# Kernel tuning notes

Measured on AMD Instinct MI355X. Metric: run time of the kernel, lower is better.

## Reference

```python
import jax, jax.numpy as jnp
import numpy as np

NUM_HEADS = 16
D_MODEL = 1024
NEG_INF = -1e30


def setup_inputs() -> dict:
    key = jax.random.key(0)
    ks = jax.random.split(key, 7)
    B, S, D = 2, 2048, D_MODEL
    scale = 1.0 / np.sqrt(D)
    return {
        "queries": jax.random.normal(ks[0], (B, S, D), dtype=jnp.float32),
        "keys": jax.random.normal(ks[1], (B, S, D), dtype=jnp.float32),
        "values": jax.random.normal(ks[2], (B, S, D), dtype=jnp.float32),
        "Wq": jax.random.normal(ks[3], (D, D), dtype=jnp.float32) * scale,
        "Wk": jax.random.normal(ks[4], (D, D), dtype=jnp.float32) * scale,
        "Wv": jax.random.normal(ks[5], (D, D), dtype=jnp.float32) * scale,
        "Wo": jax.random.normal(ks[6], (D, D), dtype=jnp.float32) * scale,
    }


def _split_heads(x, h):
    # [B, S, D] -> [B, h, S, D/h]
    B, S, D = x.shape
    return x.reshape(B, S, h, D // h).transpose(0, 2, 1, 3)


def reference(queries, keys, values, Wq, Wk, Wv, Wo):
    h = NUM_HEADS
    q = _split_heads(queries @ Wq, h)  # [B, h, S, dh]
    k = _split_heads(keys @ Wk, h)
    v = _split_heads(values @ Wv, h)
    dh = q.shape[-1]
    scores = jnp.einsum("bhqd,bhkd->bhqk", q, k) / jnp.sqrt(jnp.float32(dh))
    # original quirk: exactly-zero scores are masked to -1e30 before softmax
    scores = jnp.where(scores == 0, NEG_INF, scores)
    attn = jax.nn.softmax(scores, axis=-1)
    out = jnp.einsum("bhqk,bhkd->bhqd", attn, v)  # [B, h, S, dh]
    B, _, S, _ = out.shape
    out = out.transpose(0, 2, 1, 3).reshape(B, S, h * dh)
    return out @ Wo
```

## Files before the change

### kernel.cpp

```cpp
#include <hip/hip_runtime.h>

typedef unsigned short u16;
typedef short bf16x8 __attribute__((ext_vector_type(8)));
typedef float f32x4 __attribute__((ext_vector_type(4)));
typedef float f32x16 __attribute__((ext_vector_type(16)));

namespace {

constexpr int kB = 2, kS = 2048, kD = 1024, kH = 16, kDh = 64;
constexpr float kC2 = 0.125f * 1.44269504088896341f;

__device__ inline u16 f32_bf16(float f) {
    unsigned u = __float_as_uint(f);
    u += 0x7FFFu + ((u >> 16) & 1u);
    return (u16)(u >> 16);
}

__device__ inline float fast_exp2(float x) {
    float r;
    asm("v_exp_f32 %0, %1" : "=v"(r) : "v"(x));
    return r;
}

__device__ inline unsigned cvtpk(float a, float b) {
    unsigned r;
    asm("v_cvt_pk_bf16_f32 %0, %1, %2" : "=v"(r) : "v"(a), "v"(b));
    return r;
}

__device__ inline void plswap(unsigned& a, unsigned& b) {
    asm("v_permlane32_swap_b32 %0, %1" : "+v"(a), "+v"(b));
}

__device__ inline void gl_lds16(const void* g, void* l) {
    __builtin_amdgcn_global_load_lds(
        (const __attribute__((address_space(1))) void*)g,
        (__attribute__((address_space(3))) void*)l, 16, 0, 0);
}

__device__ inline int swz8(int l) {
    return ((l & 3) ^ ((l >> 2) & 3) ^ ((l >> 4) & 3)) * 8;
}

__global__ __launch_bounds__(256) void prep(
    const float* __restrict__ s0, const float* __restrict__ s1,
    const float* __restrict__ s2,
    u16* __restrict__ d0, u16* __restrict__ d1, u16* __restrict__ d2,
    const float* __restrict__ W0, const float* __restrict__ W1,
    const float* __restrict__ W2, const float* __restrict__ W3,
    u16* __restrict__ T0, u16* __restrict__ T1,
    u16* __restrict__ T2, u16* __restrict__ T3)
{
    const int y = blockIdx.y;
    if (y < 3) {
        const float* src = y == 0 ? s0 : (y == 1 ? s1 : s2);
        u16* dst = y == 0 ? d0 : (y == 1 ? d1 : d2);
        const int i = blockIdx.x * 256 + threadIdx.x;
        const float4* s4 = (const float4*)src;
        float4 a = s4[2 * i], b = s4[2 * i + 1];
        uint4 o;
        o.x = (unsigned)f32_bf16(a.x) | ((unsigned)f32_bf16(a.y) << 16);
        o.y = (unsigned)f32_bf16(a.z) | ((unsigned)f32_bf16(a.w) << 16);
        o.z = (unsigned)f32_bf16(b.x) | ((unsigned)f32_bf16(b.y) << 16);
        o.w = (unsigned)f32_bf16(b.z) | ((unsigned)f32_bf16(b.w) << 16);
        ((uint4*)dst)[i] = o;
        return;
    }
    if (blockIdx.x >= 256) return;
    const int z = y - 3;
    const float* W = z == 0 ? W0 : (z == 1 ? W1 : (z == 2 ? W2 : W3));
    u16* Wt = z == 0 ? T0 : (z == 1 ? T1 : (z == 2 ? T2 : T3));
    const float sc = (z == 0) ? kC2 : 1.0f;

    __shared__ __attribute__((aligned(16))) u16 T[64][65];
    const int t = threadIdx.x;
    const int n0 = (blockIdx.x & 15) * 64, k0 = (blockIdx.x >> 4) * 64;
    const int r = t >> 4, c4 = (t & 15) * 4;
#pragma unroll
    for (int it = 0; it < 4; ++it) {
        const int rr = r + 16 * it;
        float4 v = *(const float4*)(W + (size_t)(k0 + rr) * kD + n0 + c4);
        T[rr][c4 + 0] = f32_bf16(v.x * sc);
        T[rr][c4 + 1] = f32_bf16(v.y * sc);
        T[rr][c4 + 2] = f32_bf16(v.z * sc);
        T[rr][c4 + 3] = f32_bf16(v.w * sc);
    }
    __syncthreads();
#pragma unroll
    for (int it = 0; it < 4; ++it) {
        const int nn = r + 16 * it;
        uint2 pk;
        pk.x = (unsigned)T[c4 + 0][nn] | ((unsigned)T[c4 + 1][nn] << 16);
        pk.y = (unsigned)T[c4 + 2][nn] | ((unsigned)T[c4 + 3][nn] << 16);
        *(uint2*)(Wt + (size_t)(n0 + nn) * kD + k0 + c4) = pk;
    }
}

__global__ __launch_bounds__(256) void vtrans(
    const u16* __restrict__ V, u16* __restrict__ Vt)
{
    __shared__ __attribute__((aligned(16))) u16 T[64][65];
    const int t = threadIdx.x;
    const int s0 = blockIdx.x * 64;
    const int bh = blockIdx.y, b = bh >> 4, h = bh & 15;
    const int rr = t >> 3, c0 = (t & 7) * 8;
    union { u16 u[8]; uint4 v4; } buf;
#pragma unroll
    for (int p = 0; p < 2; ++p) {
        const int s = rr + 32 * p;
        buf.v4 = *(const uint4*)(V + (size_t)(b * kS + s0 + s) * kD + h * kDh + c0);
#pragma unroll
        for (int i = 0; i < 8; ++i) T[c0 + i][s] = buf.u[i];
    }
    __syncthreads();
#pragma unroll
    for (int p = 0; p < 2; ++p) {
        const int d = rr + 32 * p;
#pragma unroll
        for (int i = 0; i < 8; ++i) buf.u[i] = T[d][c0 + i];
        *(uint4*)(Vt + (size_t)(bh * kDh + d) * kS + s0 + c0) = buf.v4;
    }
}

template <bool F32OUT>
__device__ inline void gemm128_body(
    const u16* __restrict__ A, const u16* __restrict__ Wt,
    void* __restrict__ Cout, int M, int N, int K, int bx, int by)
{
    __shared__ __attribute__((aligned(16))) u16 As[128 * 32];
    __shared__ __attribute__((aligned(16))) u16 Bs[128 * 32];
    const int t = threadIdx.x, w = t >> 6, l = t & 63;
    const int quad = l >> 4, c = l & 15;
    const int wm = w >> 1, wn = w & 1;
    const int m0 = by * 128, n0 = bx * 128;
    const int lr = l >> 2, lc = swz8(l);
    const int xc = ((quad ^ (c & 3) ^ ((c >> 2) & 3))) * 8;

    const u16* ga0 = A  + (size_t)(m0 + w * 32 + lr) * K + lc;
    const u16* ga1 = A  + (size_t)(m0 + w * 32 + 16 + lr) * K + lc;
    const u16* gb0 = Wt + (size_t)(n0 + w * 32 + lr) * K + lc;
    const u16* gb1 = Wt + (size_t)(n0 + w * 32 + 16 + lr) * K + lc;
    u16* la0 = &As[(w * 32) * 32];
    u16* la1 = &As[(w * 32 + 16) * 32];
    u16* lb0 = &Bs[(w * 32) * 32];
    u16* lb1 = &Bs[(w * 32 + 16) * 32];

    f32x4 acc[4][4];
#pragma unroll
    for (int mi = 0; mi < 4; ++mi)
#pragma unroll
        for (int nj = 0; nj < 4; ++nj) acc[mi][nj] = 0;

    for (int k0 = 0; k0 < K; k0 += 32) {
        gl_lds16(ga0 + k0, la0);
        gl_lds16(ga1 + k0, la1);
        gl_lds16(gb0 + k0, lb0);
        gl_lds16(gb1 + k0, lb1);
        __syncthreads();
        bf16x8 af[4], bf[4];
#pragma unroll
        for (int mi = 0; mi < 4; ++mi)
            af[mi] = *(const bf16x8*)&As[(wm * 64 + mi * 16 + c) * 32 + xc];
#pragma unroll
        for (int nj = 0; nj < 4; ++nj)
            bf[nj] = *(const bf16x8*)&Bs[(wn * 64 + nj * 16 + c) * 32 + xc];
#pragma unroll
        for (int mi = 0; mi < 4; ++mi)
#pragma unroll
            for (int nj = 0; nj < 4; ++nj)
                acc[mi][nj] = __builtin_amdgcn_mfma_f32_16x16x32_bf16(
                    af[mi], bf[nj], acc[mi][nj], 0, 0, 0);
        __syncthreads();
    }

#pragma unroll
    for (int mi = 0; mi < 4; ++mi)
#pragma unroll
        for (int nj = 0; nj < 4; ++nj)
#pragma unroll
            for (int r = 0; r < 4; ++r) {
                const size_t row = m0 + wm * 64 + mi * 16 + quad * 4 + r;
                const size_t col = n0 + wn * 64 + nj * 16 + c;
                if (F32OUT)
                    ((float*)Cout)[row * N + col] = acc[mi][nj][r];
                else
                    ((u16*)Cout)[row * N + col] = f32_bf16(acc[mi][nj][r]);
            }
}

__global__ __launch_bounds__(256) void gemm_qkv(
    const u16* __restrict__ A0, const u16* __restrict__ A1,
    const u16* __restrict__ A2,
    const u16* __restrict__ W0, const u16* __restrict__ W1,
    const u16* __restrict__ W2,
    u16* __restrict__ C0, u16* __restrict__ C1, u16* __restrict__ C2)
{
    const int z = blockIdx.z;
    const u16* A  = z == 0 ? A0 : (z == 1 ? A1 : A2);
    const u16* Wt = z == 0 ? W0 : (z == 1 ? W1 : W2);
    u16* C = z == 0 ? C0 : (z == 1 ? C1 : C2);
    gemm128_body<false>(A, Wt, C, kB * kS, kD, kD, blockIdx.x, blockIdx.y);
}

__global__ __launch_bounds__(256) void gemm_out(
    const u16* __restrict__ A, const u16* __restrict__ Wt,
    float* __restrict__ C)
{
    __shared__ __attribute__((aligned(16))) u16 As[64 * 32];
    __shared__ __attribute__((aligned(16))) u16 Bs[128 * 32];
    const int N = kD, K = kD;
    const int t = threadIdx.x, w = t >> 6, l = t & 63;
    const int quad = l >> 4, c = l & 15;
    const int wm = w >> 1, wn = w & 1;
    const int m0 = blockIdx.y * 64, n0 = blockIdx.x * 128;
    const int lr = l >> 2, lc = swz8(l);
    const int xc = ((quad ^ (c & 3) ^ ((c >> 2) & 3))) * 8;

    const u16* ga  = A  + (size_t)(m0 + w * 16 + lr) * K + lc;
    const u16* gb0 = Wt + (size_t)(n0 + w * 16 + lr) * K + lc;
    const u16* gb1 = Wt + (size_t)(n0 + 64 + w * 16 + lr) * K + lc;
    u16* la  = &As[(w * 16) * 32];
    u16* lb0 = &Bs[(w * 16) * 32];
    u16* lb1 = &Bs[(64 + w * 16) * 32];

    f32x4 acc[2][4];
#pragma unroll
    for (int mi = 0; mi < 2; ++mi)
#pragma unroll
        for (int nj = 0; nj < 4; ++nj) acc[mi][nj] = 0;

    for (int k0 = 0; k0 < K; k0 += 32) {
        gl_lds16(ga + k0, la);
        gl_lds16(gb0 + k0, lb0);
        gl_lds16(gb1 + k0, lb1);
        __syncthreads();
        bf16x8 af[2], bf[4];
#pragma unroll
        for (int mi = 0; mi < 2; ++mi)
            af[mi] = *(const bf16x8*)&As[(wm * 32 + mi * 16 + c) * 32 + xc];
#pragma unroll
        for (int nj = 0; nj < 4; ++nj)
            bf[nj] = *(const bf16x8*)&Bs[(wn * 64 + nj * 16 + c) * 32 + xc];
#pragma unroll
        for (int mi = 0; mi < 2; ++mi)
#pragma unroll
            for (int nj = 0; nj < 4; ++nj)
                acc[mi][nj] = __builtin_amdgcn_mfma_f32_16x16x32_bf16(
                    af[mi], bf[nj], acc[mi][nj], 0, 0, 0);
        __syncthreads();
    }

#pragma unroll
    for (int mi = 0; mi < 2; ++mi)
#pragma unroll
        for (int nj = 0; nj < 4; ++nj)
#pragma unroll
            for (int r = 0; r < 4; ++r) {
                const size_t row = m0 + wm * 32 + mi * 16 + quad * 4 + r;
                const size_t col = n0 + wn * 64 + nj * 16 + c;
                C[row * N + col] = acc[mi][nj][r];
            }
}

__global__ __launch_bounds__(256) void attn(
    const u16* __restrict__ Q, const u16* __restrict__ K,
    const u16* __restrict__ Vt, u16* __restrict__ AO)
{
    __shared__ __attribute__((aligned(16))) u16 KsA[64 * 64];
    __shared__ __attribute__((aligned(16))) u16 KsB[64 * 64];
    __shared__ __attribute__((aligned(16))) u16 VtA[64 * 64];
    __shared__ __attribute__((aligned(16))) u16 VtB[64 * 64];

    const int t = threadIdx.x, w = t >> 6, l = t & 63;
    const int half = l >> 5, m = l & 31;
    const int wgid = blockIdx.x;
    const int xcd = wgid & 7, idx = wgid >> 3;
    const int bh = xcd + 8 * (idx & 3);
    const int q0 = (idx >> 2) * 128;
    const int b = bh >> 4, h = bh & 15;
    const int sr = l >> 3;
    const int sc = (l & 7) ^ sr;

    const size_t kbase = (size_t)(b * kS) * kD + h * kDh;
    const size_t vbase = (size_t)bh * kDh * kS;

    auto stage = [&](int kt, u16* KsP, u16* VtP) {
#pragma unroll
        for (int i = 0; i < 2; ++i) {
            const int R0 = w * 16 + i * 8;
            gl_lds16(K + kbase + (size_t)(kt * 64 + R0 + sr) * kD + sc * 8,
                     &KsP[R0 * 64]);
            gl_lds16(Vt + vbase + (size_t)(R0 + sr) * kS + kt * 64 + sc * 8,
                     &VtP[R0 * 64]);
        }
    };

    stage(0, KsA, VtA);

    bf16x8 qf[4];
    {
        const u16* qp = Q + (size_t)(b * kS + q0 + w * 32 + m) * kD
                        + h * kDh + half * 8;
#pragma unroll
        for (int ch = 0; ch < 4; ++ch)
            qf[ch] = *(const bf16x8*)(qp + ch * 16);
    }

    bf16x8 ones;
#pragma unroll
    for (int i = 0; i < 8; ++i) ones[i] = (short)0x3F80;

    f32x16 o0 = 0, o1 = 0;
    f32x16 ol = 0;

    __syncthreads();

    auto compute = [&](const u16* KsP, const u16* VtP) {
        f32x16 s0 = 0, s1 = 0;
        __builtin_amdgcn_s_setprio(1);
#pragma unroll
        for (int ch = 0; ch < 4; ++ch) {
            const int xo = ((2 * ch + half) ^ (m & 7)) * 8;
            const bf16x8 kf0 = *(const bf16x8*)&KsP[(m) * 64 + xo];
            const bf16x8 kf1 = *(const bf16x8*)&KsP[(32 + m) * 64 + xo];
            s0 = __builtin_amdgcn_mfma_f32_32x32x16_bf16(kf0, qf[ch], s0, 0, 0, 0);
            s1 = __builtin_amdgcn_mfma_f32_32x32x16_bf16(kf1, qf[ch], s1, 0, 0, 0);
        }
        __builtin_amdgcn_s_setprio(0);
#pragma unroll
        for (int r = 0; r < 16; ++r) {
            s0[r] = fast_exp2(s0[r]);
            s1[r] = fast_exp2(s1[r]);
        }
        __builtin_amdgcn_s_setprio(1);
#pragma unroll
        for (int ts = 0; ts < 4; ++ts) {
            const int rb = (ts & 1) * 8;
            unsigned c0, c1, c2, c3;
            if (ts < 2) {
                c0 = cvtpk(s0[rb + 0], s0[rb + 1]);
                c1 = cvtpk(s0[rb + 2], s0[rb + 3]);
                c2 = cvtpk(s0[rb + 4], s0[rb + 5]);
                c3 = cvtpk(s0[rb + 6], s0[rb + 7]);
            } else {
                c0 = cvtpk(s1[rb + 0], s1[rb + 1]);
                c1 = cvtpk(s1[rb + 2], s1[rb + 3]);
                c2 = cvtpk(s1[rb + 4], s1[rb + 5]);
                c3 = cvtpk(s1[rb + 6], s1[rb + 7]);
            }
            plswap(c0, c2);
            plswap(c1, c3);
            union { unsigned u[4]; bf16x8 v; } pb;
            pb.u[0] = c0; pb.u[1] = c1; pb.u[2] = c2; pb.u[3] = c3;
            const int xo = ((2 * ts + half) ^ (m & 7)) * 8;
            const bf16x8 vf0 = *(const bf16x8*)&VtP[(m) * 64 + xo];
            const bf16x8 vf1 = *(const bf16x8*)&VtP[(32 + m) * 64 + xo];
            o0 = __builtin_amdgcn_mfma_f32_32x32x16_bf16(vf0, pb.v, o0, 0, 0, 0);
            o1 = __builtin_amdgcn_mfma_f32_32x32x16_bf16(vf1, pb.v, o1, 0, 0, 0);
            ol = __builtin_amdgcn_mfma_f32_32x32x16_bf16(ones, pb.v, ol, 0, 0, 0);
        }
        __builtin_amdgcn_s_setprio(0);
    };

    constexpr int NT = kS / 64;
#pragma unroll 1
    for (int kt = 0; kt < NT; kt += 2) {
        if (kt + 1 < NT) stage(kt + 1, KsB, VtB);
        compute(KsA, VtA);
        __syncthreads();
        if (kt + 2 < NT) stage(kt + 2, KsA, VtA);
        compute(KsB, VtB);
        __syncthreads();
    }

    const float inv = 1.0f / ol[0];

    u16* ob = w == 0 ? KsA : (w == 1 ? KsB : (w == 2 ? VtA : VtB));
#pragma unroll
    for (int r = 0; r < 4; ++r) {
        uint2 p0, p1;
        p0.x = cvtpk(o0[4 * r + 0] * inv, o0[4 * r + 1] * inv);
        p0.y = cvtpk(o0[4 * r + 2] * inv, o0[4 * r + 3] * inv);
        p1.x = cvtpk(o1[4 * r + 0] * inv, o1[4 * r + 1] * inv);
        p1.y = cvtpk(o1[4 * r + 2] * inv, o1[4 * r + 3] * inv);
        *(uint2*)&ob[m * 64 + ((r ^ (m & 7)) << 3) + 4 * half] = p0;
        *(uint2*)&ob[m * 64 + (((4 + r) ^ (m & 7)) << 3) + 4 * half] = p1;
    }
    const size_t obase = (size_t)(b * kS + q0 + w * 32) * kD + h * kDh;
#pragma unroll
    for (int i = 0; i < 4; ++i) {
        const int q = l >> 1;
        const int tt = (l & 1) + i * 2;
        uint4 dd = *(const uint4*)&ob[q * 64 + ((tt ^ (q & 7)) << 3)];
        *(uint4*)(AO + obase + (size_t)q * kD + tt * 8) = dd;
    }
}

}

extern "C" void kernel_launch(void* const* d_in, const int* in_sizes, int n_in,
                              void* d_out, int out_size, void* d_ws, size_t ws_size,
                              hipStream_t stream)
{
    const float* q_in = (const float*)d_in[0];
    const float* k_in = (const float*)d_in[1];
    const float* v_in = (const float*)d_in[2];
    const float* Wq   = (const float*)d_in[3];
    const float* Wk   = (const float*)d_in[4];
    const float* Wv   = (const float*)d_in[5];
    const float* Wo   = (const float*)d_in[6];

    u16* ws = (u16*)d_ws;
    const size_t M1 = 1u << 20;
    u16* xq  = ws;
    u16* xk  = ws + 4 * M1;
    u16* xv  = ws + 8 * M1;
    u16* Wtq = ws + 12 * M1;
    u16* Wtk = ws + 13 * M1;
    u16* Wtv = ws + 14 * M1;
    u16* Wto = ws + 15 * M1;
    u16* Qp  = ws + 16 * M1;
    u16* Kp  = ws + 20 * M1;
    u16* Vp  = ws + 24 * M1;
    u16* AO  = ws + 28 * M1;
    u16* Vtg = xq;

    hipLaunchKernelGGL(prep, dim3(2048, 7), dim3(256), 0, stream,
                       q_in, k_in, v_in, xq, xk, xv,
                       Wq, Wk, Wv, Wo, Wtq, Wtk, Wtv, Wto);

    hipLaunchKernelGGL(gemm_qkv, dim3(8, 32, 3), dim3(256), 0, stream,
                       xq, xk, xv, Wtq, Wtk, Wtv, Qp, Kp, Vp);

    hipLaunchKernelGGL(vtrans, dim3(32, 32), dim3(256), 0, stream, Vp, Vtg);

    hipLaunchKernelGGL(attn, dim3(512), dim3(256), 0, stream, Qp, Kp, Vtg, AO);

    hipLaunchKernelGGL(gemm_out, dim3(8, 64), dim3(256), 0, stream,
                       AO, Wto, (float*)d_out);
}
```

Measured before the change: 217.2 us.

## Fuse V transpose into QKV GEMM epilogue and reswizzle attention LDS tiles

The separate vtrans kernel is removed. The V-projection blocks of gemm_qkv now transpose their accumulator tile through shared memory and write V directly in the [bh, d, s] layout that attention reads. This saves one launch and one round trip of V through global memory, at the cost of extra LDS in the GEMM, which may lower its occupancy. The attention kernel's K/Vt LDS swizzle also now XORs in the row-group bits, meant to reduce bank conflicts on the fragment reads.

```diff
diff --git a/kernel.cpp b/kernel.cpp
--- a/kernel.cpp
+++ b/kernel.cpp
@@ -96,43 +96,25 @@
     }
 }
 
-__global__ __launch_bounds__(256) void vtrans(
-    const u16* __restrict__ V, u16* __restrict__ Vt)
-{
-    __shared__ __attribute__((aligned(16))) u16 T[64][65];
-    const int t = threadIdx.x;
-    const int s0 = blockIdx.x * 64;
-    const int bh = blockIdx.y, b = bh >> 4, h = bh & 15;
-    const int rr = t >> 3, c0 = (t & 7) * 8;
-    union { u16 u[8]; uint4 v4; } buf;
-#pragma unroll
-    for (int p = 0; p < 2; ++p) {
-        const int s = rr + 32 * p;
-        buf.v4 = *(const uint4*)(V + (size_t)(b * kS + s0 + s) * kD + h * kDh + c0);
-#pragma unroll
-        for (int i = 0; i < 8; ++i) T[c0 + i][s] = buf.u[i];
-    }
-    __syncthreads();
-#pragma unroll
-    for (int p = 0; p < 2; ++p) {
-        const int d = rr + 32 * p;
-#pragma unroll
-        for (int i = 0; i < 8; ++i) buf.u[i] = T[d][c0 + i];
-        *(uint4*)(Vt + (size_t)(bh * kDh + d) * kS + s0 + c0) = buf.v4;
-    }
-}
-
-template <bool F32OUT>
-__device__ inline void gemm128_body(
-    const u16* __restrict__ A, const u16* __restrict__ Wt,
-    void* __restrict__ Cout, int M, int N, int K, int bx, int by)
+__global__ __launch_bounds__(256) void gemm_qkv(
+    const u16* __restrict__ A0, const u16* __restrict__ A1,
+    const u16* __restrict__ A2,
+    const u16* __restrict__ W0, const u16* __restrict__ W1,
+    const u16* __restrict__ W2,
+    u16* __restrict__ C0, u16* __restrict__ C1, u16* __restrict__ Vt)
 {
     __shared__ __attribute__((aligned(16))) u16 As[128 * 32];
     __shared__ __attribute__((aligned(16))) u16 Bs[128 * 32];
+    __shared__ __attribute__((aligned(16))) u16 Tt[64][136];
+    const int N = kD, K = kD;
+    const int z = blockIdx.z;
+    const u16* A  = z == 0 ? A0 : (z == 1 ? A1 : A2);
+    const u16* Wt = z == 0 ? W0 : (z == 1 ? W1 : W2);
+
     const int t = threadIdx.x, w = t >> 6, l = t & 63;
     const int quad = l >> 4, c = l & 15;
     const int wm = w >> 1, wn = w & 1;
-    const int m0 = by * 128, n0 = bx * 128;
+    const int m0 = blockIdx.y * 128, n0 = blockIdx.x * 128;
     const int lr = l >> 2, lc = swz8(l);
     const int xc = ((quad ^ (c & 3) ^ ((c >> 2) & 3))) * 8;
 
@@ -173,33 +155,45 @@
         __syncthreads();
     }
 
-#pragma unroll
-    for (int mi = 0; mi < 4; ++mi)
-#pragma unroll
-        for (int nj = 0; nj < 4; ++nj)
-#pragma unroll
-            for (int r = 0; r < 4; ++r) {
-                const size_t row = m0 + wm * 64 + mi * 16 + quad * 4 + r;
-                const size_t col = n0 + wn * 64 + nj * 16 + c;
-                if (F32OUT)
-                    ((float*)Cout)[row * N + col] = acc[mi][nj][r];
-                else
-                    ((u16*)Cout)[row * N + col] = f32_bf16(acc[mi][nj][r]);
-            }
-}
-
-__global__ __launch_bounds__(256) void gemm_qkv(
-    const u16* __restrict__ A0, const u16* __restrict__ A1,
-    const u16* __restrict__ A2,
-    const u16* __restrict__ W0, const u16* __restrict__ W1,
-    const u16* __restrict__ W2,
-    u16* __restrict__ C0, u16* __restrict__ C1, u16* __restrict__ C2)
-{
-    const int z = blockIdx.z;
-    const u16* A  = z == 0 ? A0 : (z == 1 ? A1 : A2);
-    const u16* Wt = z == 0 ? W0 : (z == 1 ? W1 : W2);
-    u16* C = z == 0 ? C0 : (z == 1 ? C1 : C2);
-    gemm128_body<false>(A, Wt, C, kB * kS, kD, kD, blockIdx.x, blockIdx.y);
+    if (z < 2) {
+        u16* C = z == 0 ? C0 : C1;
+#pragma unroll
+        for (int mi = 0; mi < 4; ++mi)
+#pragma unroll
+            for (int nj = 0; nj < 4; ++nj)
+#pragma unroll
+                for (int r = 0; r < 4; ++r) {
+                    const size_t row = m0 + wm * 64 + mi * 16 + quad * 4 + r;
+                    const size_t col = n0 + wn * 64 + nj * 16 + c;
+                    C[row * N + col] = f32_bf16(acc[mi][nj][r]);
+                }
+        return;
+    }
+    const int srow = m0 & 2047;
+    const int bbase = (m0 >> 11) << 4;
+#pragma unroll 1
+    for (int p = 0; p < 2; ++p) {
+        if (wn == p) {
+#pragma unroll
+            for (int mi = 0; mi < 4; ++mi)
+#pragma unroll
+                for (int nj = 0; nj < 4; ++nj)
+#pragma unroll
+                    for (int r = 0; r < 4; ++r)
+                        Tt[nj * 16 + c][wm * 64 + mi * 16 + quad * 4 + r] =
+                            f32_bf16(acc[mi][nj][r]);
+        }
+        __syncthreads();
+        const size_t vb = (size_t)(bbase + blockIdx.x * 2 + p) * (kDh * kS);
+        const int s8 = t & 15, dbase = t >> 4;
+#pragma unroll
+        for (int dd = 0; dd < 4; ++dd) {
+            const int d = dbase + dd * 16;
+            uint4 v = *(const uint4*)&Tt[d][s8 * 8];
+            *(uint4*)(Vt + vb + (size_t)d * kS + srow + s8 * 8) = v;
+        }
+        __syncthreads();
+    }
 }
 
 __global__ __launch_bounds__(256) void gemm_out(
@@ -279,7 +273,6 @@
     const int q0 = (idx >> 2) * 128;
     const int b = bh >> 4, h = bh & 15;
     const int sr = l >> 3;
-    const int sc = (l & 7) ^ sr;
 
     const size_t kbase = (size_t)(b * kS) * kD + h * kDh;
     const size_t vbase = (size_t)bh * kDh * kS;
@@ -288,6 +281,7 @@
 #pragma unroll
         for (int i = 0; i < 2; ++i) {
             const int R0 = w * 16 + i * 8;
+            const int sc = (l & 7) ^ sr ^ (w * 2 + i);
             gl_lds16(K + kbase + (size_t)(kt * 64 + R0 + sr) * kD + sc * 8,
                      &KsP[R0 * 64]);
             gl_lds16(Vt + vbase + (size_t)(R0 + sr) * kS + kt * 64 + sc * 8,
@@ -320,9 +314,9 @@
         __builtin_amdgcn_s_setprio(1);
 #pragma unroll
         for (int ch = 0; ch < 4; ++ch) {
-            const int xo = ((2 * ch + half) ^ (m & 7)) * 8;
+            const int xo = ((2 * ch + half) ^ (m & 7) ^ (m >> 3)) * 8;
             const bf16x8 kf0 = *(const bf16x8*)&KsP[(m) * 64 + xo];
-            const bf16x8 kf1 = *(const bf16x8*)&KsP[(32 + m) * 64 + xo];
+            const bf16x8 kf1 = *(const bf16x8*)&KsP[(32 + m) * 64 + (xo ^ 32)];
             s0 = __builtin_amdgcn_mfma_f32_32x32x16_bf16(kf0, qf[ch], s0, 0, 0, 0);
             s1 = __builtin_amdgcn_mfma_f32_32x32x16_bf16(kf1, qf[ch], s1, 0, 0, 0);
         }
@@ -352,9 +346,9 @@
             plswap(c1, c3);
             union { unsigned u[4]; bf16x8 v; } pb;
             pb.u[0] = c0; pb.u[1] = c1; pb.u[2] = c2; pb.u[3] = c3;
-            const int xo = ((2 * ts + half) ^ (m & 7)) * 8;
+            const int xo = ((2 * ts + half) ^ (m & 7) ^ (m >> 3)) * 8;
             const bf16x8 vf0 = *(const bf16x8*)&VtP[(m) * 64 + xo];
-            const bf16x8 vf1 = *(const bf16x8*)&VtP[(32 + m) * 64 + xo];
+            const bf16x8 vf1 = *(const bf16x8*)&VtP[(32 + m) * 64 + (xo ^ 32)];
             o0 = __builtin_amdgcn_mfma_f32_32x32x16_bf16(vf0, pb.v, o0, 0, 0, 0);
             o1 = __builtin_amdgcn_mfma_f32_32x32x16_bf16(vf1, pb.v, o1, 0, 0, 0);
             ol = __builtin_amdgcn_mfma_f32_32x32x16_bf16(ones, pb.v, ol, 0, 0, 0);
@@ -421,20 +415,17 @@
     u16* Wto = ws + 15 * M1;
     u16* Qp  = ws + 16 * M1;
     u16* Kp  = ws + 20 * M1;
-    u16* Vp  = ws + 24 * M1;
+    u16* Vt  = ws + 24 * M1;
     u16* AO  = ws + 28 * M1;
-    u16* Vtg = xq;
 
     hipLaunchKernelGGL(prep, dim3(2048, 7), dim3(256), 0, stream,
                        q_in, k_in, v_in, xq, xk, xv,
                        Wq, Wk, Wv, Wo, Wtq, Wtk, Wtv, Wto);
 
     hipLaunchKernelGGL(gemm_qkv, dim3(8, 32, 3), dim3(256), 0, stream,
-                       xq, xk, xv, Wtq, Wtk, Wtv, Qp, Kp, Vp);
-
-    hipLaunchKernelGGL(vtrans, dim3(32, 32), dim3(256), 0, stream, Vp, Vtg);
-
-    hipLaunchKernelGGL(attn, dim3(512), dim3(256), 0, stream, Qp, Kp, Vtg, AO);
+                       xq, xk, xv, Wtq, Wtk, Wtv, Qp, Kp, Vt);
+
+    hipLaunchKernelGGL(attn, dim3(512), dim3(256), 0, stream, Qp, Kp, Vt, AO);
 
     hipLaunchKernelGGL(gemm_out, dim3(8, 64), dim3(256), 0, stream,
                        AO, Wto, (float*)d_out);
```

After: 235.5 us. +8.4%, slower.
